# Performance work log

Measured on AMD Instinct MI355X. Metric: run time of the kernel, lower is better.

## Reference

```python
import jax, jax.numpy as jnp
import numpy as np

N = 50000
E = 800000
IN = 256
OUT = 32
H1 = 8
NEG_SLOPE = 0.2


def setup_inputs() -> dict:
    key = jax.random.key(0)
    ks = jax.random.split(key, 12)
    x = jax.random.normal(ks[0], (N, IN), dtype=jnp.float32)
    src = jax.random.randint(ks[1], (E,), 0, N, dtype=jnp.int32)
    dst = jax.random.randint(ks[2], (E,), 0, N, dtype=jnp.int32)
    s1 = 1.0 / np.sqrt(IN)
    s2 = 1.0 / np.sqrt(H1 * OUT)
    # layer 1 (8 heads, residual = Identity since IN == H1*OUT)
    W1 = jax.random.normal(ks[3], (IN, H1 * OUT), dtype=jnp.float32) * s1
    al1 = jax.random.normal(ks[4], (H1, OUT), dtype=jnp.float32) * s1
    ar1 = jax.random.normal(ks[5], (H1, OUT), dtype=jnp.float32) * s1
    b1 = jnp.zeros((H1 * OUT,), dtype=jnp.float32)
    # layer 2 (1 head, residual = Linear since H1*OUT != OUT)
    W2 = jax.random.normal(ks[6], (H1 * OUT, OUT), dtype=jnp.float32) * s2
    al2 = jax.random.normal(ks[7], (1, OUT), dtype=jnp.float32) * s2
    ar2 = jax.random.normal(ks[8], (1, OUT), dtype=jnp.float32) * s2
    resW2 = jax.random.normal(ks[9], (H1 * OUT, OUT), dtype=jnp.float32) * s2
    b2 = jnp.zeros((OUT,), dtype=jnp.float32)
    return {"x": x, "src": src, "dst": dst, "W1": W1, "al1": al1, "ar1": ar1,
            "b1": b1, "W2": W2, "al2": al2, "ar2": ar2, "resW2": resW2, "b2": b2}


def gat_layer(x, src, dst, W, al, ar, bias, heads, out_feats, res_fn):
    # x: (N, in). feat: (N, H, D)
    feat = (x @ W).reshape(N, heads, out_feats)
    el = jnp.sum(feat * al[None], axis=-1)  # (N, H)
    er = jnp.sum(feat * ar[None], axis=-1)  # (N, H)
    e = jax.nn.leaky_relu(el[src] + er[dst], NEG_SLOPE)  # (E, H)
    # edge softmax over incoming edges of each destination node
    emax = jax.ops.segment_max(e, dst, num_segments=N)  # (N, H)
    ee = jnp.exp(e - emax[dst])
    esum = jax.ops.segment_sum(ee, dst, num_segments=N)  # (N, H)
    a = ee / esum[dst]  # (E, H)
    # gather-multiply-scatter-add aggregation
    msg = feat[src] * a[..., None]  # (E, H, D)
    rst = jax.ops.segment_sum(msg, dst, num_segments=N)  # (N, H, D)
    rst = rst + res_fn(x)
    rst = rst + bias.reshape(1, heads, out_feats)
    return rst


def reference(x, src, dst, W1, al1, ar1, b1, W2, al2, ar2, resW2, b2):
    # layer 1: 8 heads, residual Identity (IN == H1*OUT)
    y = gat_layer(x, src, dst, W1, al1, ar1, b1, H1, OUT,
                  lambda h: h.reshape(N, H1, OUT))
    y = jax.nn.relu(y).reshape(N, H1 * OUT)
    # layer 2: 1 head, residual Linear projection
    y = gat_layer(y, src, dst, W2, al2, ar2, b2, 1, OUT,
                  lambda h: (h @ resW2).reshape(N, 1, OUT))
    return y
```

## Files before the change

### kernel.cpp

```cpp
#include <hip/hip_runtime.h>
#include <hip/hip_bf16.h>
#include <hip/hip_fp8.h>

#define N_NODES 50000
#define M_PAD   50048
#define N_EDGES 800000
#define NEG_SLOPE 0.2f

#define EPT 8
#define BKA 391
#define NBUCK 256
#define NPB 196
#define SEGCAP 40
#define GBLK 782
#define APAD 264

typedef __attribute__((ext_vector_type(8))) short bf16x8;
typedef __attribute__((ext_vector_type(4))) float f32x4;
typedef __attribute__((ext_vector_type(2))) float f32x2;

__device__ __forceinline__ unsigned short f2bf(float f) {
    unsigned u = __float_as_uint(f);
    u += 0x7FFFu + ((u >> 16) & 1u);
    return (unsigned short)(u >> 16);
}
__device__ __forceinline__ float bf2f(unsigned short h) {
    return __uint_as_float(((unsigned)h) << 16);
}

#if __has_builtin(__builtin_amdgcn_cvt_pk_f32_fp8)
__device__ __forceinline__ f32x2 fp8pk_lo(unsigned int p) { return __builtin_amdgcn_cvt_pk_f32_fp8(p, false); }
__device__ __forceinline__ f32x2 fp8pk_hi(unsigned int p) { return __builtin_amdgcn_cvt_pk_f32_fp8(p, true); }
#else
__device__ __forceinline__ float fp82f_s(unsigned char b) {
    __hip_fp8_e4m3 t; t.__x = (__hip_fp8_storage_t)b; return (float)t;
}
__device__ __forceinline__ f32x2 fp8pk_lo(unsigned int p) {
    f32x2 r; r.x = fp82f_s(p & 0xff); r.y = fp82f_s((p >> 8) & 0xff); return r;
}
__device__ __forceinline__ f32x2 fp8pk_hi(unsigned int p) {
    f32x2 r; r.x = fp82f_s((p >> 16) & 0xff); r.y = fp82f_s(p >> 24); return r;
}
#endif

#if __has_builtin(__builtin_amdgcn_cvt_pk_fp8_f32)
__device__ __forceinline__ unsigned int fp8enc2(float a, float b) {
    return (unsigned int)__builtin_amdgcn_cvt_pk_fp8_f32(a, b, 0, false);
}
#else
__device__ __forceinline__ unsigned int fp8enc2(float a, float b) {
    __hip_fp8_e4m3 ta(a), tb(b);
    return (unsigned int)ta.__x | ((unsigned int)tb.__x << 8);
}
#endif


__global__ __launch_bounds__(256) void k_trans(const float* __restrict__ W1, const float* __restrict__ W2,
                                               const float* __restrict__ resW2, const float* __restrict__ x,
                                               unsigned short* __restrict__ W1F, unsigned short* __restrict__ W2T,
                                               unsigned short* __restrict__ xb, unsigned int* __restrict__ btot) {
    int flat = blockIdx.y * 10 + blockIdx.x;
    if (flat == 0) btot[threadIdx.x] = 0;

    if (blockIdx.y < 8) {
        __shared__ unsigned short tile[32][33];
        int bx = blockIdx.x;
        const float* in;
        int Nn, n0;
        if (bx < 8)      { in = W1;    Nn = 256; n0 = bx * 32; }
        else if (bx == 8){ in = W2;    Nn = 32;  n0 = 0; }
        else             { in = resW2; Nn = 32;  n0 = 0; }
        int k0 = blockIdx.y * 32;
        int tx = threadIdx.x & 31, ty = threadIdx.x >> 5;
        #pragma unroll
        for (int r = 0; r < 4; ++r) {
            int k = k0 + ty + r * 8;
            tile[ty + r * 8][tx] = f2bf(in[(size_t)k * Nn + n0 + tx]);
        }
        __syncthreads();
        #pragma unroll
        for (int r = 0; r < 4; ++r) {
            int n = ty + r * 8;
            unsigned short val = tile[tx][n];
            int col = n0 + n;
            int kk = k0 + tx;
            if (bx < 8) {
                size_t idx = (((size_t)(col >> 4) * 8 + (kk >> 5)) << 9)
                           + ((((kk >> 3) & 3) * 16 + (col & 15)) << 3) + (kk & 7);
                W1F[idx] = val;
            } else {
                unsigned short* out = (bx == 8) ? W2T : (W2T + 32 * 256);
                out[(size_t)col * 256 + kk] = val;
            }
        }
    } else {
        int xid = flat - 80;
        const size_t NCHUNK = (size_t)M_PAD * 256 / 8;
        for (size_t c = (size_t)xid * 256 + threadIdx.x; c < NCHUNK; c += (size_t)720 * 256) {
            size_t base = c * 8;
            float4 a = make_float4(0.f, 0.f, 0.f, 0.f), b = a;
            if (base < (size_t)N_NODES * 256) {
                a = *(const float4*)(x + base);
                b = *(const float4*)(x + base + 4);
            }
            ushort4 h0, h1;
            h0.x = f2bf(a.x); h0.y = f2bf(a.y); h0.z = f2bf(a.z); h0.w = f2bf(a.w);
            h1.x = f2bf(b.x); h1.y = f2bf(b.y); h1.z = f2bf(b.z); h1.w = f2bf(b.w);
            *(ushort4*)(xb + base) = h0;
            *(ushort4*)(xb + base + 4) = h1;
        }
    }
}


__global__ __launch_bounds__(512) void k_gemm1(const unsigned short* __restrict__ xb,
                                               const unsigned short* __restrict__ W1F,
                                               const float* __restrict__ al1, const float* __restrict__ ar1,
                                               unsigned char* __restrict__ Cb8,
                                               float* __restrict__ el1, float* __restrict__ er1) {
    __shared__ unsigned short sA[64 * APAD];
    const int t = threadIdx.x;
    const int bm0 = blockIdx.x * 64;
    const int wave = t >> 6, lane = t & 63;
    const int wm = (wave & 1) * 32, wn = (wave >> 1) * 64;
    const int lm = lane & 15, quad = lane >> 4;

    #pragma unroll
    for (int rr = 0; rr < 4; ++rr) {
        int ch = rr * 512 + t;
        int row = ch >> 5, w = ch & 31;
        bf16x8 vv = *(const bf16x8*)(xb + (size_t)(bm0 + row) * 256 + w * 8);
        *(bf16x8*)(sA + row * APAD + w * 8) = vv;
    }
    __syncthreads();

    f32x4 acc[2][4];
    #pragma unroll
    for (int i = 0; i < 2; ++i)
        #pragma unroll
        for (int j = 0; j < 4; ++j)
            #pragma unroll
            for (int r = 0; r < 4; ++r) acc[i][j][r] = 0.f;

    const unsigned short* bp[4];
    #pragma unroll
    for (int i = 0; i < 4; ++i)
        bp[i] = W1F + ((size_t)((wave >> 1) * 4 + i)) * 4096 + lane * 8;
    const unsigned short* ap[2];
    #pragma unroll
    for (int i = 0; i < 2; ++i)
        ap[i] = sA + (wm + i * 16 + lm) * APAD + quad * 8;

    bf16x8 nb[4];
    #pragma unroll
    for (int i = 0; i < 4; ++i) nb[i] = *(const bf16x8*)(bp[i]);

    #pragma unroll
    for (int q = 0; q < 8; ++q) {
        bf16x8 cb[4];
        #pragma unroll
        for (int i = 0; i < 4; ++i) cb[i] = nb[i];
        if (q < 7) {
            #pragma unroll
            for (int i = 0; i < 4; ++i) nb[i] = *(const bf16x8*)(bp[i] + (q + 1) * 512);
        }
        bf16x8 ca[2];
        #pragma unroll
        for (int i = 0; i < 2; ++i) ca[i] = *(const bf16x8*)(ap[i] + q * 32);
        #pragma unroll
        for (int mi = 0; mi < 2; ++mi)
            #pragma unroll
            for (int ni = 0; ni < 4; ++ni)
                acc[mi][ni] = __builtin_amdgcn_mfma_f32_16x16x32_bf16(ca[mi], cb[ni], acc[mi][ni], 0, 0, 0);
    }

    #pragma unroll
    for (int mi = 0; mi < 2; ++mi) {
        #pragma unroll
        for (int ni = 0; ni < 4; ++ni) {
            int col = wn + ni * 16 + lm;
            int row0 = bm0 + wm + mi * 16 + quad * 4;
            unsigned int p01 = fp8enc2(acc[mi][ni][0], acc[mi][ni][1]);
            unsigned int p23 = fp8enc2(acc[mi][ni][2], acc[mi][ni][3]);
            Cb8[(size_t)(row0 + 0) * 256 + col] = (unsigned char)(p01 & 0xff);
            Cb8[(size_t)(row0 + 1) * 256 + col] = (unsigned char)((p01 >> 8) & 0xff);
            Cb8[(size_t)(row0 + 2) * 256 + col] = (unsigned char)(p23 & 0xff);
            Cb8[(size_t)(row0 + 3) * 256 + col] = (unsigned char)((p23 >> 8) & 0xff);
        }
    }
    float alv[4], arv[4];
    #pragma unroll
    for (int ni = 0; ni < 4; ++ni) {
        int colg = wn + ni * 16 + lm;
        alv[ni] = al1[colg];
        arv[ni] = ar1[colg];
    }
    int head0 = wn >> 5;
    #pragma unroll
    for (int gg = 0; gg < 2; ++gg) {
        #pragma unroll
        for (int mi = 0; mi < 2; ++mi) {
            #pragma unroll
            for (int r = 0; r < 4; ++r) {
                float pel = acc[mi][2 * gg][r] * alv[2 * gg] + acc[mi][2 * gg + 1][r] * alv[2 * gg + 1];
                float per = acc[mi][2 * gg][r] * arv[2 * gg] + acc[mi][2 * gg + 1][r] * arv[2 * gg + 1];
                #pragma unroll
                for (int m = 1; m <= 8; m <<= 1) {
                    pel += __shfl_xor(pel, m, 64);
                    per += __shfl_xor(per, m, 64);
                }
                if (lm == 0) {
                    int row = bm0 + wm + mi * 16 + quad * 4 + r;
                    el1[row * 8 + head0 + gg] = pel;
                    er1[row * 8 + head0 + gg] = per;
                }
            }
        }
    }
}


__global__ __launch_bounds__(256) void k_bucketA(const int* __restrict__ src, const int* __restrict__ dst,
                                                 uint2* __restrict__ seg, unsigned int* __restrict__ cnt,
                                                 unsigned int* __restrict__ btot) {
    __shared__ unsigned int lcnt[NBUCK];
    int vb = blockIdx.x;
    lcnt[threadIdx.x] = 0;
    __syncthreads();
    int base = vb * (256 * EPT) + threadIdx.x;
    int sv[EPT], dv[EPT], bk[EPT], lr[EPT];
    #pragma unroll
    for (int q = 0; q < EPT; ++q) {
        int i = base + q * 256;
        if (i < N_EDGES) { sv[q] = src[i]; dv[q] = dst[i]; }
        else dv[q] = -1;
    }
    #pragma unroll
    for (int q = 0; q < EPT; ++q) {
        if (dv[q] >= 0) {
            bk[q] = (int)((unsigned)dv[q] / NPB);
            lr[q] = atomicAdd(&lcnt[bk[q]], 1u);
        }
    }
    __syncthreads();
    cnt[vb * NBUCK + threadIdx.x] = lcnt[threadIdx.x];
    if (lcnt[threadIdx.x] > 0) atomicAdd(&btot[threadIdx.x], lcnt[threadIdx.x]);
    #pragma unroll
    for (int q = 0; q < EPT; ++q) {
        if (dv[q] >= 0 && lr[q] < SEGCAP) {
            size_t slot = ((size_t)bk[q] * BKA + vb) * SEGCAP + lr[q];
            seg[slot] = make_uint2((unsigned)sv[q], (unsigned)dv[q] - (unsigned)bk[q] * NPB);
        }
    }
}


__global__ __launch_bounds__(256) void k_bucketB(const uint2* __restrict__ seg, const unsigned int* __restrict__ cnt,
                                                 const unsigned int* __restrict__ btot,
                                                 int* __restrict__ rowoff, int* __restrict__ csr_src) {
    __shared__ unsigned int hist[NPB];
    __shared__ unsigned int cursor[NPB];
    __shared__ unsigned int red[256];
    int b = blockIdx.x;
    int t = threadIdx.x;
    if (t < NPB) hist[t] = 0;
    red[t] = (t < b) ? btot[t] : 0;
    __syncthreads();
    #pragma unroll
    for (int off = 128; off > 0; off >>= 1) {
        if (t < off) red[t] += red[t + off];
        __syncthreads();
    }
    unsigned int base = red[0];
    __syncthreads();
    for (int s = t; s < BKA; s += 256) {
        unsigned int c = cnt[s * NBUCK + b];
        const uint2* sp = seg + ((size_t)b * BKA + s) * SEGCAP;
        for (unsigned int j = 0; j < c; ++j) {
            atomicAdd(&hist[sp[j].y], 1u);
        }
    }
    __syncthreads();
    red[t] = (t < NPB) ? hist[t] : 0;
    __syncthreads();
    for (int off = 1; off < 256; off <<= 1) {
        unsigned int val = (t >= off) ? red[t - off] : 0;
        __syncthreads();
        red[t] += val;
        __syncthreads();
    }
    if (t < NPB) {
        unsigned int excl = red[t] - hist[t];
        cursor[t] = excl;
        int v = b * NPB + t;
        if (v < N_NODES) rowoff[v] = (int)(base + excl);
    }
    if (b == NBUCK - 1 && t == 0) rowoff[N_NODES] = N_EDGES;
    __syncthreads();
    for (int s = t; s < BKA; s += 256) {
        unsigned int c = cnt[s * NBUCK + b];
        const uint2* sp = seg + ((size_t)b * BKA + s) * SEGCAP;
        for (unsigned int j = 0; j < c; ++j) {
            uint2 eg = sp[j];
            unsigned int r = atomicAdd(&cursor[eg.y], 1u);
            csr_src[base + r] = (int)eg.x;
        }
    }
}


__global__ __launch_bounds__(256) void k_agg1(const unsigned char* __restrict__ feat8,
                                              const float* __restrict__ el1, const float* __restrict__ er1,
                                              const unsigned short* __restrict__ xb, const float* __restrict__ b1,
                                              const int* __restrict__ rowoff, const int* __restrict__ csr_src,
                                              unsigned short* __restrict__ y_b) {
    int v = (blockIdx.x * 256 + threadIdx.x) >> 6;
    int lane = threadIdx.x & 63;
    if (v >= M_PAD) return;
    int c0 = lane * 4;
    if (v >= N_NODES) {
        ushort4 z = {0, 0, 0, 0};
        *(ushort4*)(y_b + (size_t)v * 256 + c0) = z;
        return;
    }
    int h = lane >> 3;
    float er  = er1[v * 8 + h];
    float erc = er1[v * 8 + (lane & 7)];
    float ax = 0.f, ay = 0.f, az = 0.f, aw = 0.f, wsum = 0.f;
    int s = rowoff[v], e = rowoff[v + 1];
    int j = s;
    for (; j + 7 < e; j += 8) {
        int um = csr_src[j + (lane >> 3)];
        float elv = el1[um * 8 + (lane & 7)];
        int u[8];
        #pragma unroll
        for (int q = 0; q < 8; ++q) u[q] = __shfl(um, q * 8);
        unsigned int hv[8];
        #pragma unroll
        for (int q = 0; q < 8; ++q) hv[q] = *(const unsigned int*)(feat8 + (size_t)u[q] * 256 + c0);
        float tq = elv + erc;
        tq = fmaxf(tq, NEG_SLOPE * tq);
        float wv = __expf(tq);
        #pragma unroll
        for (int q = 0; q < 8; ++q) {
            float w = __shfl(wv, q * 8 + h);
            wsum += w;
            f32x2 lo = fp8pk_lo(hv[q]);
            f32x2 hi = fp8pk_hi(hv[q]);
            ax += w * lo.x; ay += w * lo.y; az += w * hi.x; aw += w * hi.y;
        }
    }
    for (; j + 3 < e; j += 4) {
        int u[4];
        #pragma unroll
        for (int q = 0; q < 4; ++q) u[q] = csr_src[j + q];
        float tt[4];
        #pragma unroll
        for (int q = 0; q < 4; ++q) tt[q] = el1[u[q] * 8 + h] + er;
        unsigned int hv[4];
        #pragma unroll
        for (int q = 0; q < 4; ++q) hv[q] = *(const unsigned int*)(feat8 + (size_t)u[q] * 256 + c0);
        #pragma unroll
        for (int q = 0; q < 4; ++q) {
            float tq = fmaxf(tt[q], NEG_SLOPE * tt[q]);
            float w = __expf(tq);
            wsum += w;
            f32x2 lo = fp8pk_lo(hv[q]);
            f32x2 hi = fp8pk_hi(hv[q]);
            ax += w * lo.x; ay += w * lo.y; az += w * hi.x; aw += w * hi.y;
        }
    }
    for (; j < e; ++j) {
        int u = csr_src[j];
        float tt = el1[u * 8 + h] + er;
        unsigned int hh = *(const unsigned int*)(feat8 + (size_t)u * 256 + c0);
        tt = fmaxf(tt, NEG_SLOPE * tt);
        float w = __expf(tt);
        wsum += w;
        f32x2 lo = fp8pk_lo(hh);
        f32x2 hi = fp8pk_hi(hh);
        ax += w * lo.x; ay += w * lo.y; az += w * hi.x; aw += w * hi.y;
    }
    float inv = (e > s) ? 1.f / wsum : 0.f;
    ushort4 rh = *(const ushort4*)(xb + (size_t)v * 256 + c0);
    float4 bb = *(const float4*)(b1 + c0);
    ushort4 o;
    o.x = f2bf(fmaxf(ax * inv + bf2f(rh.x) + bb.x, 0.f));
    o.y = f2bf(fmaxf(ay * inv + bf2f(rh.y) + bb.y, 0.f));
    o.z = f2bf(fmaxf(az * inv + bf2f(rh.z) + bb.z, 0.f));
    o.w = f2bf(fmaxf(aw * inv + bf2f(rh.w) + bb.w, 0.f));
    *(ushort4*)(y_b + (size_t)v * 256 + c0) = o;
}


__global__ __launch_bounds__(256) void k_gemm2f(const unsigned short* __restrict__ Ab,
                                                const unsigned short* __restrict__ BT,
                                                const float* __restrict__ al2, const float* __restrict__ ar2,
                                                unsigned short* __restrict__ feat2b, float* __restrict__ res2,
                                                float* __restrict__ el2, float* __restrict__ er2) {
    const int t = threadIdx.x;
    const int bm0 = blockIdx.x * 64;
    const int wave = t >> 6, lane = t & 63;
    const int wm = (wave & 1) * 32, wn = (wave >> 1) * 32;
    const int lm = lane & 15, quad = lane >> 4;

    f32x4 acc[2][2];
    #pragma unroll
    for (int i = 0; i < 2; ++i)
        #pragma unroll
        for (int j = 0; j < 2; ++j)
            #pragma unroll
            for (int r = 0; r < 4; ++r) acc[i][j][r] = 0.f;

    const unsigned short* bp[2];
    const unsigned short* ap[2];
    #pragma unroll
    for (int i = 0; i < 2; ++i) {
        bp[i] = BT + (size_t)(wn + i * 16 + lm) * 256 + quad * 8;
        ap[i] = Ab + (size_t)(bm0 + wm + i * 16 + lm) * 256 + quad * 8;
    }

    bf16x8 nb[2], na[2];
    #pragma unroll
    for (int i = 0; i < 2; ++i) { nb[i] = *(const bf16x8*)(bp[i]); na[i] = *(const bf16x8*)(ap[i]); }

    #pragma unroll
    for (int k0 = 0; k0 < 256; k0 += 32) {
        bf16x8 cb[2], ca[2];
        #pragma unroll
        for (int i = 0; i < 2; ++i) { cb[i] = nb[i]; ca[i] = na[i]; }
        if (k0 + 32 < 256) {
            #pragma unroll
            for (int i = 0; i < 2; ++i) {
                nb[i] = *(const bf16x8*)(bp[i] + k0 + 32);
                na[i] = *(const bf16x8*)(ap[i] + k0 + 32);
            }
        }
        #pragma unroll
        for (int mi = 0; mi < 2; ++mi)
            #pragma unroll
            for (int ni = 0; ni < 2; ++ni)
                acc[mi][ni] = __builtin_amdgcn_mfma_f32_16x16x32_bf16(ca[mi], cb[ni], acc[mi][ni], 0, 0, 0);
    }

    #pragma unroll
    for (int mi = 0; mi < 2; ++mi) {
        #pragma unroll
        for (int ni = 0; ni < 2; ++ni) {
            int col = wn + ni * 16 + lm;
            #pragma unroll
            for (int r = 0; r < 4; ++r) {
                int row = bm0 + wm + mi * 16 + quad * 4 + r;
                float val = acc[mi][ni][r];
                if (col < 32) feat2b[(size_t)row * 32 + col] = f2bf(val);
                else          res2[(size_t)row * 32 + col - 32] = val;
            }
        }
    }
    if (wn == 0) {
        float alv[2], arv[2];
        #pragma unroll
        for (int ni = 0; ni < 2; ++ni) {
            alv[ni] = al2[ni * 16 + lm];
            arv[ni] = ar2[ni * 16 + lm];
        }
        #pragma unroll
        for (int mi = 0; mi < 2; ++mi) {
            #pragma unroll
            for (int r = 0; r < 4; ++r) {
                float pel = acc[mi][0][r] * alv[0] + acc[mi][1][r] * alv[1];
                float per = acc[mi][0][r] * arv[0] + acc[mi][1][r] * arv[1];
                #pragma unroll
                for (int m = 1; m <= 8; m <<= 1) {
                    pel += __shfl_xor(pel, m, 64);
                    per += __shfl_xor(per, m, 64);
                }
                if (lm == 0) {
                    int row = bm0 + wm + mi * 16 + quad * 4 + r;
                    el2[row] = pel;
                    er2[row] = per;
                }
            }
        }
    }
}


__global__ __launch_bounds__(256) void k_agg2(const unsigned short* __restrict__ feat2b,
                                              const float* __restrict__ el2, const float* __restrict__ er2,
                                              const float* __restrict__ res2, const float* __restrict__ b2,
                                              const int* __restrict__ rowoff, const int* __restrict__ csr_src,
                                              float* __restrict__ out) {
    int g = blockIdx.x * 256 + threadIdx.x;
    int v = g >> 5;
    int c = g & 31;
    if (v >= N_NODES) return;
    float er = er2[v];
    float acc = 0.f, wsum = 0.f;
    int s = rowoff[v], e = rowoff[v + 1];
    int j = s;
    for (; j + 3 < e; j += 4) {
        int u[4];
        #pragma unroll
        for (int q = 0; q < 4; ++q) u[q] = csr_src[j + q];
        float tt[4];
        #pragma unroll
        for (int q = 0; q < 4; ++q) tt[q] = el2[u[q]] + er;
        unsigned short fv[4];
        #pragma unroll
        for (int q = 0; q < 4; ++q) fv[q] = feat2b[(size_t)u[q] * 32 + c];
        #pragma unroll
        for (int q = 0; q < 4; ++q) {
            float tq = fmaxf(tt[q], NEG_SLOPE * tt[q]);
            float w = __expf(tq);
            wsum += w;
            acc += w * bf2f(fv[q]);
        }
    }
    for (; j < e; ++j) {
        int u = csr_src[j];
        float t = el2[u] + er;
        t = fmaxf(t, NEG_SLOPE * t);
        float w = __expf(t);
        wsum += w;
        acc += w * bf2f(feat2b[(size_t)u * 32 + c]);
    }
    float inv = (e > s) ? 1.f / wsum : 0.f;
    out[(size_t)v * 32 + c] = acc * inv + res2[(size_t)v * 32 + c] + b2[c];
}


extern "C" void kernel_launch(void* const* d_in, const int* in_sizes, int n_in,
                              void* d_out, int out_size, void* d_ws, size_t ws_size,
                              hipStream_t stream) {
    const float* x     = (const float*)d_in[0];
    const int*   src   = (const int*)d_in[1];
    const int*   dst   = (const int*)d_in[2];
    const float* W1    = (const float*)d_in[3];
    const float* al1   = (const float*)d_in[4];
    const float* ar1   = (const float*)d_in[5];
    const float* b1    = (const float*)d_in[6];
    const float* W2    = (const float*)d_in[7];
    const float* al2   = (const float*)d_in[8];
    const float* ar2   = (const float*)d_in[9];
    const float* resW2 = (const float*)d_in[10];
    const float* b2    = (const float*)d_in[11];
    float* out = (float*)d_out;

    char* ws = (char*)d_ws;
    size_t off = 0;
    auto alloc = [&](size_t bytes) {
        void* p = ws + off;
        off += (bytes + 255) & ~(size_t)255;
        return p;
    };
    unsigned short* xb     = (unsigned short*)alloc((size_t)M_PAD * 256 * 2);
    unsigned char*  feat8  = (unsigned char*)alloc((size_t)M_PAD * 256);
    unsigned short* y_b    = (unsigned short*)alloc((size_t)M_PAD * 256 * 2);
    unsigned short* W1F    = (unsigned short*)alloc((size_t)256 * 256 * 2);
    unsigned short* W2T    = (unsigned short*)alloc((size_t)64 * 256 * 2);
    unsigned short* feat2b = (unsigned short*)alloc((size_t)M_PAD * 32 * 2);
    float* res2   = (float*)alloc((size_t)M_PAD * 32 * 4);
    float* el1    = (float*)alloc((size_t)M_PAD * 8 * 4);
    float* er1    = (float*)alloc((size_t)M_PAD * 8 * 4);
    float* el2    = (float*)alloc((size_t)M_PAD * 4);
    float* er2    = (float*)alloc((size_t)M_PAD * 4);
    int*   rowoff = (int*)alloc((size_t)(N_NODES + 1) * 4);
    int*   csr    = (int*)alloc((size_t)N_EDGES * 4);
    uint2* seg    = (uint2*)alloc((size_t)NBUCK * BKA * SEGCAP * 8);
    unsigned int* cnt  = (unsigned int*)alloc((size_t)BKA * NBUCK * 4);
    unsigned int* btot = (unsigned int*)alloc((size_t)NBUCK * 4);
    (void)ws_size;

    k_trans<<<dim3(10, 80), 256, 0, stream>>>(W1, W2, resW2, x, W1F, W2T, xb, btot);

    k_bucketA<<<BKA, 256, 0, stream>>>(src, dst, seg, cnt, btot);

    k_gemm1<<<GBLK, 512, 0, stream>>>(xb, W1F, al1, ar1, feat8, el1, er1);

    k_bucketB<<<NBUCK, 256, 0, stream>>>(seg, cnt, btot, rowoff, csr);

    k_agg1<<<(M_PAD * 64) / 256, 256, 0, stream>>>(feat8, el1, er1, xb, b1, rowoff, csr, y_b);

    k_gemm2f<<<M_PAD / 64, 256, 0, stream>>>(y_b, W2T, al2, ar2, feat2b, res2, el2, er2);
    k_agg2<<<(N_NODES * 32) / 256, 256, 0, stream>>>(feat2b, el2, er2, res2, b2, rowoff, csr, out);
}
```

Measured before the change: 251.0 us.

## Fuse independent preprocessing kernels into combined launches

Merges the weight/input conversion kernel with edge bucketing (phase A) into one launch, and the first GEMM with CSR construction (phase B) into another. Independent work then runs concurrently across CUs, and two kernel launches and their tail gaps go away. The btot zeroing moves to a memset before the fused kernel. Bucket B now runs with 512-thread blocks where half the threads idle in the scans, and LDS use per block rises from the shared allocations.

```diff
diff --git a/kernel.cpp b/kernel.cpp
--- a/kernel.cpp
+++ b/kernel.cpp
@@ -14,6 +14,8 @@
 #define SEGCAP 40
 #define GBLK 782
 #define APAD 264
+#define FUSE1_T (800 + BKA)
+#define FUSE2_T (GBLK + NBUCK)
 
 typedef __attribute__((ext_vector_type(8))) short bf16x8;
 typedef __attribute__((ext_vector_type(4))) float f32x4;
@@ -55,22 +57,56 @@
 #endif
 
 
-__global__ __launch_bounds__(256) void k_trans(const float* __restrict__ W1, const float* __restrict__ W2,
+__global__ __launch_bounds__(256) void k_fuse1(const float* __restrict__ W1, const float* __restrict__ W2,
                                                const float* __restrict__ resW2, const float* __restrict__ x,
+                                               const int* __restrict__ src, const int* __restrict__ dst,
                                                unsigned short* __restrict__ W1F, unsigned short* __restrict__ W2T,
-                                               unsigned short* __restrict__ xb, unsigned int* __restrict__ btot) {
-    int flat = blockIdx.y * 10 + blockIdx.x;
-    if (flat == 0) btot[threadIdx.x] = 0;
-
-    if (blockIdx.y < 8) {
+                                               unsigned short* __restrict__ xb,
+                                               uint2* __restrict__ seg, unsigned int* __restrict__ cnt,
+                                               unsigned int* __restrict__ btot) {
+    int bid = blockIdx.x;
+    if (bid >= 800) {
+        __shared__ unsigned int lcnt[NBUCK];
+        int vb = bid - 800;
+        lcnt[threadIdx.x] = 0;
+        __syncthreads();
+        int base = vb * (256 * EPT) + threadIdx.x;
+        int sv[EPT], dv[EPT], bk[EPT], lr[EPT];
+        #pragma unroll
+        for (int q = 0; q < EPT; ++q) {
+            int i = base + q * 256;
+            if (i < N_EDGES) { sv[q] = src[i]; dv[q] = dst[i]; }
+            else dv[q] = -1;
+        }
+        #pragma unroll
+        for (int q = 0; q < EPT; ++q) {
+            if (dv[q] >= 0) {
+                bk[q] = (int)((unsigned)dv[q] / NPB);
+                lr[q] = atomicAdd(&lcnt[bk[q]], 1u);
+            }
+        }
+        __syncthreads();
+        cnt[vb * NBUCK + threadIdx.x] = lcnt[threadIdx.x];
+        if (lcnt[threadIdx.x] > 0) atomicAdd(&btot[threadIdx.x], lcnt[threadIdx.x]);
+        #pragma unroll
+        for (int q = 0; q < EPT; ++q) {
+            if (dv[q] >= 0 && lr[q] < SEGCAP) {
+                size_t slot = ((size_t)bk[q] * BKA + vb) * SEGCAP + lr[q];
+                seg[slot] = make_uint2((unsigned)sv[q], (unsigned)dv[q] - (unsigned)bk[q] * NPB);
+            }
+        }
+        return;
+    }
+    int flat = bid;
+    if (flat < 80) {
         __shared__ unsigned short tile[32][33];
-        int bx = blockIdx.x;
+        int bx = flat % 10;
         const float* in;
         int Nn, n0;
         if (bx < 8)      { in = W1;    Nn = 256; n0 = bx * 32; }
         else if (bx == 8){ in = W2;    Nn = 32;  n0 = 0; }
         else             { in = resW2; Nn = 32;  n0 = 0; }
-        int k0 = blockIdx.y * 32;
+        int k0 = (flat / 10) * 32;
         int tx = threadIdx.x & 31, ty = threadIdx.x >> 5;
         #pragma unroll
         for (int r = 0; r < 4; ++r) {
@@ -113,14 +149,15 @@
 }
 
 
-__global__ __launch_bounds__(512) void k_gemm1(const unsigned short* __restrict__ xb,
-                                               const unsigned short* __restrict__ W1F,
-                                               const float* __restrict__ al1, const float* __restrict__ ar1,
-                                               unsigned char* __restrict__ Cb8,
-                                               float* __restrict__ el1, float* __restrict__ er1) {
+__device__ __forceinline__ void gemm1_body(int gblk,
+                                           const unsigned short* __restrict__ xb,
+                                           const unsigned short* __restrict__ W1F,
+                                           const float* __restrict__ al1, const float* __restrict__ ar1,
+                                           unsigned char* __restrict__ Cb8,
+                                           float* __restrict__ el1, float* __restrict__ er1) {
     __shared__ unsigned short sA[64 * APAD];
     const int t = threadIdx.x;
-    const int bm0 = blockIdx.x * 64;
+    const int bm0 = gblk * 64;
     const int wave = t >> 6, lane = t & 63;
     const int wm = (wave & 1) * 32, wn = (wave >> 1) * 64;
     const int lm = lane & 15, quad = lane >> 4;
@@ -220,51 +257,26 @@
 }
 
 
-__global__ __launch_bounds__(256) void k_bucketA(const int* __restrict__ src, const int* __restrict__ dst,
-                                                 uint2* __restrict__ seg, unsigned int* __restrict__ cnt,
-                                                 unsigned int* __restrict__ btot) {
-    __shared__ unsigned int lcnt[NBUCK];
-    int vb = blockIdx.x;
-    lcnt[threadIdx.x] = 0;
-    __syncthreads();
-    int base = vb * (256 * EPT) + threadIdx.x;
-    int sv[EPT], dv[EPT], bk[EPT], lr[EPT];
-    #pragma unroll
-    for (int q = 0; q < EPT; ++q) {
-        int i = base + q * 256;
-        if (i < N_EDGES) { sv[q] = src[i]; dv[q] = dst[i]; }
-        else dv[q] = -1;
-    }
-    #pragma unroll
-    for (int q = 0; q < EPT; ++q) {
-        if (dv[q] >= 0) {
-            bk[q] = (int)((unsigned)dv[q] / NPB);
-            lr[q] = atomicAdd(&lcnt[bk[q]], 1u);
-        }
-    }
-    __syncthreads();
-    cnt[vb * NBUCK + threadIdx.x] = lcnt[threadIdx.x];
-    if (lcnt[threadIdx.x] > 0) atomicAdd(&btot[threadIdx.x], lcnt[threadIdx.x]);
-    #pragma unroll
-    for (int q = 0; q < EPT; ++q) {
-        if (dv[q] >= 0 && lr[q] < SEGCAP) {
-            size_t slot = ((size_t)bk[q] * BKA + vb) * SEGCAP + lr[q];
-            seg[slot] = make_uint2((unsigned)sv[q], (unsigned)dv[q] - (unsigned)bk[q] * NPB);
-        }
-    }
-}
-
-
-__global__ __launch_bounds__(256) void k_bucketB(const uint2* __restrict__ seg, const unsigned int* __restrict__ cnt,
-                                                 const unsigned int* __restrict__ btot,
-                                                 int* __restrict__ rowoff, int* __restrict__ csr_src) {
+__global__ __launch_bounds__(512) void k_fuse2(const unsigned short* __restrict__ xb,
+                                               const unsigned short* __restrict__ W1F,
+                                               const float* __restrict__ al1, const float* __restrict__ ar1,
+                                               unsigned char* __restrict__ Cb8,
+                                               float* __restrict__ el1, float* __restrict__ er1,
+                                               const uint2* __restrict__ seg, const unsigned int* __restrict__ cnt,
+                                               const unsigned int* __restrict__ btot,
+                                               int* __restrict__ rowoff, int* __restrict__ csr_src) {
+    int bid = blockIdx.x;
+    if (bid < GBLK) {
+        gemm1_body(bid, xb, W1F, al1, ar1, Cb8, el1, er1);
+        return;
+    }
     __shared__ unsigned int hist[NPB];
     __shared__ unsigned int cursor[NPB];
     __shared__ unsigned int red[256];
-    int b = blockIdx.x;
+    int b = bid - GBLK;
     int t = threadIdx.x;
     if (t < NPB) hist[t] = 0;
-    red[t] = (t < b) ? btot[t] : 0;
+    if (t < 256) red[t] = (t < b) ? btot[t] : 0;
     __syncthreads();
     #pragma unroll
     for (int off = 128; off > 0; off >>= 1) {
@@ -273,7 +285,7 @@
     }
     unsigned int base = red[0];
     __syncthreads();
-    for (int s = t; s < BKA; s += 256) {
+    for (int s = t; s < BKA; s += 512) {
         unsigned int c = cnt[s * NBUCK + b];
         const uint2* sp = seg + ((size_t)b * BKA + s) * SEGCAP;
         for (unsigned int j = 0; j < c; ++j) {
@@ -281,12 +293,12 @@
         }
     }
     __syncthreads();
-    red[t] = (t < NPB) ? hist[t] : 0;
+    if (t < 256) red[t] = (t < NPB) ? hist[t] : 0;
     __syncthreads();
     for (int off = 1; off < 256; off <<= 1) {
-        unsigned int val = (t >= off) ? red[t - off] : 0;
+        unsigned int val = (t >= off && t < 256) ? red[t - off] : 0u;
         __syncthreads();
-        red[t] += val;
+        if (t < 256) red[t] += val;
         __syncthreads();
     }
     if (t < NPB) {
@@ -297,7 +309,7 @@
     }
     if (b == NBUCK - 1 && t == 0) rowoff[N_NODES] = N_EDGES;
     __syncthreads();
-    for (int s = t; s < BKA; s += 256) {
+    for (int s = t; s < BKA; s += 512) {
         unsigned int c = cnt[s * NBUCK + b];
         const uint2* sp = seg + ((size_t)b * BKA + s) * SEGCAP;
         for (unsigned int j = 0; j < c; ++j) {
@@ -572,13 +584,11 @@
     unsigned int* btot = (unsigned int*)alloc((size_t)NBUCK * 4);
     (void)ws_size;
 
-    k_trans<<<dim3(10, 80), 256, 0, stream>>>(W1, W2, resW2, x, W1F, W2T, xb, btot);
-
-    k_bucketA<<<BKA, 256, 0, stream>>>(src, dst, seg, cnt, btot);
-
-    k_gemm1<<<GBLK, 512, 0, stream>>>(xb, W1F, al1, ar1, feat8, el1, er1);
-
-    k_bucketB<<<NBUCK, 256, 0, stream>>>(seg, cnt, btot, rowoff, csr);
+    hipMemsetAsync(btot, 0, (size_t)NBUCK * 4, stream);
+
+    k_fuse1<<<FUSE1_T, 256, 0, stream>>>(W1, W2, resW2, x, src, dst, W1F, W2T, xb, seg, cnt, btot);
+
+    k_fuse2<<<FUSE2_T, 512, 0, stream>>>(xb, W1F, al1, ar1, feat8, el1, er1, seg, cnt, btot, rowoff, csr);
 
     k_agg1<<<(M_PAD * 64) / 256, 256, 0, stream>>>(feat8, el1, er1, xb, b1, rowoff, csr, y_b);
 
```

After: 245.8 us. -2.1%, faster.
